# Performance work log

Hardware: AMD Instinct MI355X
Metric: run time of the kernel (lower is better)

Reference implementation:

```python
import jax, jax.numpy as jnp
import numpy as np

B, CIN, COUT, K, H, W, NPTS = 8, 256, 256, 4, 128, 128, 512


def setup_inputs() -> dict:
    key = jax.random.key(0)
    ks = jax.random.split(key, 9)
    inp = {
        'input': jax.random.normal(ks[0], (B, CIN, H, W), dtype=jnp.float32),
        'ax': jax.random.uniform(ks[1], (B, NPTS), dtype=jnp.float32) * (W - 1),
        'ay': jax.random.uniform(ks[2], (B, NPTS), dtype=jnp.float32) * (H - 1),
        # 1x1 conv = matmul over channels
        'Wp': jax.random.normal(ks[3], (COUT, CIN), dtype=jnp.float32) * 0.02,
        'bp': jnp.zeros((COUT,), dtype=jnp.float32),
        'Woff': jax.random.normal(ks[4], (K, 2, CIN), dtype=jnp.float32) * 0.02,
        'boff': jnp.zeros((K, 2), dtype=jnp.float32),
        'Ww': jax.random.normal(ks[5], (K, CIN), dtype=jnp.float32) * 0.02,
        'bw': jnp.zeros((K,), dtype=jnp.float32),
    }
    return inp


def _bilinear_zeros(img, xs, ys):
    """grid_sample(mode='bilinear', padding_mode='zeros').
    img: [b, C, H, W]; xs, ys: [b, H, W] source pixel coords. Returns [b, H, W, C]."""
    b, C, h, w = img.shape
    img_hwc = jnp.transpose(img, (0, 2, 3, 1))  # [b, H, W, C]
    x0 = jnp.floor(xs)
    y0 = jnp.floor(ys)
    wx1 = xs - x0
    wy1 = ys - y0
    bidx = jnp.arange(b)[:, None, None]

    def corner(xi, yi, wgt):
        valid = (xi >= 0) & (xi < w) & (yi >= 0) & (yi < h)
        xc = jnp.clip(xi, 0, w - 1).astype(jnp.int32)
        yc = jnp.clip(yi, 0, h - 1).astype(jnp.int32)
        v = img_hwc[bidx, yc, xc]  # [b, H, W, C]
        return v * (jnp.where(valid, wgt, 0.0))[..., None]

    out = (corner(x0, y0, (1 - wx1) * (1 - wy1))
           + corner(x0 + 1, y0, wx1 * (1 - wy1))
           + corner(x0, y0 + 1, (1 - wx1) * wy1)
           + corner(x0 + 1, y0 + 1, wx1 * wy1))
    return out


def _forward(input, ax, ay, Wp, bp, Woff, boff, Ww, bw):
    b, c, h, w = input.shape
    k = Ww.shape[0]
    proj = jnp.einsum('bchw,oc->bohw', input, Wp) + bp[None, :, None, None]
    # k flow fields [k, b, 2, h, w]
    flows = jnp.einsum('bchw,koc->kbohw', input, Woff) + boff[:, None, :, None, None]
    logits = jnp.einsum('bchw,kc->bkhw', input, Ww) + bw[None, :, None, None]
    wts = jax.nn.softmax(logits, axis=1)  # [b, k, h, w]

    gx = jnp.arange(w, dtype=input.dtype)[None, None, :]
    gy = jnp.arange(h, dtype=input.dtype)[None, :, None]
    # torch normalization: n = 2*v/(dim-1)-1, then grid_sample(align_corners=False)
    # maps n -> ((n+1)*dim - 1)/2 = v*dim/(dim-1) - 0.5
    sx_scale = w / max(w - 1, 1)
    sy_scale = h / max(h - 1, 1)

    # gather sum_k wts_k * sampled_k at every pixel (loop over small fixed k)
    summed = jnp.zeros((b, h, w, proj.shape[1]), dtype=input.dtype)
    for i in range(k):
        sx = (gx + flows[i, :, 0]) * sx_scale - 0.5  # [b, h, w]
        sy = (gy + flows[i, :, 1]) * sy_scale - 0.5
        summed = summed + wts[:, i, :, :, None] * _bilinear_zeros(proj, sx, sy)

    # point gather: feat[num, :, id[1], id[0]] with id = trunc((ax, ay))
    ix = jnp.trunc(ax).astype(jnp.int32)  # width index
    iy = jnp.trunc(ay).astype(jnp.int32)  # height index
    out = summed[jnp.arange(b)[:, None], iy, ix]  # [b, num_pts, out_ch]
    return out


def reference(input, ax, ay, Wp, bp, Woff, boff, Ww, bw):
    return _forward(input, ax, ay, Wp, bp, Woff, boff, Ww, bw)
```

## Files before the change

### kernel.cpp

```cpp
#include <hip/hip_runtime.h>
#include <hip/hip_fp16.h>

#define B_      8
#define CIN_    256
#define COUT_   256
#define K_      4
#define H_      128
#define W_      128
#define NPTS_   512

#define NPTS_TOT_   (B_ * NPTS_)
#define T_BYTES_    ((size_t)B_ * H_ * W_ * CIN_ * sizeof(__half))
#define WTS_OFF_    T_BYTES_
#define SITES_OFF_  (WTS_OFF_   + (size_t)NPTS_TOT_ * 16 * 4)
#define WSUM_OFF_   (SITES_OFF_ + (size_t)NPTS_TOT_ * 16 * 4)
#define WS_NEED_    (WSUM_OFF_  + (size_t)NPTS_TOT_ * 4)

__global__ __launch_bounds__(256) void ka_kernel(
    const float* __restrict__ input,
    const float* __restrict__ ax,
    const float* __restrict__ ay,
    const float* __restrict__ Woff,
    const float* __restrict__ boff,
    const float* __restrict__ Ww,
    const float* __restrict__ bw,
    __half* __restrict__ T,
    float* __restrict__ wts_g,
    int*   __restrict__ sites_g,
    float* __restrict__ wsums_g)
{
    __shared__ float lt[32][129];
    __shared__ float xs[CIN_];
    __shared__ float dotv[12];
    __shared__ float wc16[16];

    const int bid = blockIdx.x;
    const int t   = threadIdx.x;

    if (bid < 8192) {
        const int b   = bid >> 10;
        const int r   = bid & 1023;
        const int h   = r >> 3;
        const int c0  = (r & 7) << 5;

        const int c = t >> 3;
        const int m = t & 7;
        const float* __restrict__ src = input + (((size_t)(b * CIN_ + c0 + c) * H_ + h) * W_);
        #pragma unroll
        for (int q = 0; q < 4; ++q) {
            const int w = m * 4 + q * 32;
            const float4 v = *reinterpret_cast<const float4*>(src + w);
            lt[c][w]     = v.x;
            lt[c][w + 1] = v.y;
            lt[c][w + 2] = v.z;
            lt[c][w + 3] = v.w;
        }
        __syncthreads();

        const int wph = t >> 2;
        const int j0  = (t & 3) << 3;
        #pragma unroll
        for (int g = 0; g < 2; ++g) {
            const int w = wph + (g << 6);
            unsigned int words[4];
            #pragma unroll
            for (int i = 0; i < 4; ++i) {
                __half2 h2 = __floats2half2_rn(lt[j0 + 2 * i][w], lt[j0 + 2 * i + 1][w]);
                words[i] = *reinterpret_cast<unsigned int*>(&h2);
            }
            __half* dst = T + (((size_t)(b * H_ + h) * W_ + w) * CIN_ + c0 + j0);
            *reinterpret_cast<uint4*>(dst) = make_uint4(words[0], words[1], words[2], words[3]);
        }
        return;
    }

    const int pt = bid - 8192;
    const int b  = pt >> 9;

    const int ix = (int)truncf(ax[pt]);
    const int iy = (int)truncf(ay[pt]);
    const float* __restrict__ chan = input + (size_t)b * (CIN_ * H_ * W_) + (size_t)t * (H_ * W_);

    xs[t] = chan[iy * W_ + ix];
    __syncthreads();

    const int wave = t >> 6;
    const int lane = t & 63;
    #pragma unroll
    for (int r = 0; r < 3; ++r) {
        const int d = wave * 3 + r;
        const float* __restrict__ row = (d < 8) ? (Woff + d * CIN_) : (Ww + (d - 8) * CIN_);
        float s = 0.f;
        #pragma unroll
        for (int q = 0; q < 4; ++q) {
            const int c = lane + q * 64;
            s = fmaf(xs[c], row[c], s);
        }
        #pragma unroll
        for (int off = 32; off > 0; off >>= 1)
            s += __shfl_down(s, off);
        if (lane == 0) dotv[d] = s;
    }
    __syncthreads();

    if (t < 4) {
        const int k = t;
        const float l0 = dotv[8]  + bw[0];
        const float l1 = dotv[9]  + bw[1];
        const float l2 = dotv[10] + bw[2];
        const float l3 = dotv[11] + bw[3];
        const float mx = fmaxf(fmaxf(l0, l1), fmaxf(l2, l3));
        const float e0 = expf(l0 - mx), e1 = expf(l1 - mx);
        const float e2 = expf(l2 - mx), e3 = expf(l3 - mx);
        const float ek = (k == 0) ? e0 : (k == 1) ? e1 : (k == 2) ? e2 : e3;
        const float wk = ek / (e0 + e1 + e2 + e3);

        const float scale = 128.0f / 127.0f;
        const float fx = dotv[2 * k]     + boff[2 * k];
        const float fy = dotv[2 * k + 1] + boff[2 * k + 1];
        const float sxv = ((float)ix + fx) * scale - 0.5f;
        const float syv = ((float)iy + fy) * scale - 0.5f;
        const float x0f = floorf(sxv), y0f = floorf(syv);
        const float wx1 = sxv - x0f, wy1 = syv - y0f;
        const int x0 = (int)x0f, y0 = (int)y0f;
        #pragma unroll
        for (int ci = 0; ci < 4; ++ci) {
            const int xi = x0 + (ci & 1);
            const int yi = y0 + (ci >> 1);
            const bool valid = (xi >= 0) & (xi < W_) & (yi >= 0) & (yi < H_);
            float wc = ((ci & 1) ? wx1 : 1.f - wx1) * ((ci >> 1) ? wy1 : 1.f - wy1) * wk;
            wc = valid ? wc : 0.f;
            const int xc = min(max(xi, 0), W_ - 1);
            const int yc = min(max(yi, 0), H_ - 1);
            const int idx = k * 4 + ci;
            wc16[idx] = wc;
            wts_g[pt * 16 + idx]   = wc;
            sites_g[pt * 16 + idx] = ((b * H_ + yc) * W_ + xc) * CIN_;
        }
    }
    __syncthreads();
    if (t == 0) {
        float s = 0.f;
        #pragma unroll
        for (int i = 0; i < 16; ++i) s += wc16[i];
        wsums_g[pt] = s;
    }
}

__global__ __launch_bounds__(512) void kb_kernel(
    const __half* __restrict__ T,
    const float* __restrict__ Wp,
    const float* __restrict__ bp,
    const float* __restrict__ wts_g,
    const int*   __restrict__ sites_g,
    const float* __restrict__ wsums_g,
    float* __restrict__ out)
{
    __shared__ float xsh[16][260];
    __shared__ float wtile[32 * 256];
    __shared__ float swts[16][16];
    __shared__ int   ssites[16][16];
    __shared__ float swsum[16];

    const int blk = blockIdx.x;
    const int p0g = blk << 4;
    const int tid = threadIdx.x;

    if (tid < 256) {
        swts[tid >> 4][tid & 15]   = wts_g[p0g * 16 + tid];
        ssites[tid >> 4][tid & 15] = sites_g[p0g * 16 + tid];
    } else if (tid < 256 + 16) {
        swsum[tid - 256] = wsums_g[p0g + (tid - 256)];
    }
    __syncthreads();

    {
        const int p   = tid >> 5;
        const int oct = tid & 31;
        const int c0  = oct << 3;
        float a[8] = {0.f, 0.f, 0.f, 0.f, 0.f, 0.f, 0.f, 0.f};
        #pragma unroll
        for (int s = 0; s < 16; ++s) {
            const float w = swts[p][s];
            const uint4 raw = *reinterpret_cast<const uint4*>(T + (size_t)ssites[p][s] + c0);
            const __half* hh = reinterpret_cast<const __half*>(&raw);
            #pragma unroll
            for (int j = 0; j < 8; ++j)
                a[j] = fmaf(w, __half2float(hh[j]), a[j]);
        }
        *reinterpret_cast<float4*>(&xsh[p][c0])     = make_float4(a[0], a[1], a[2], a[3]);
        *reinterpret_cast<float4*>(&xsh[p][c0 + 4]) = make_float4(a[4], a[5], a[6], a[7]);
    }
    __syncthreads();

    const int oq = tid & 63;
    const int pp = tid >> 6;
    const int o0 = oq << 2;
    const int p0 = pp << 1;

    const float4 bpv = *reinterpret_cast<const float4*>(bp + o0);
    const float ws0 = swsum[p0], ws1 = swsum[p0 + 1];
    float a00 = bpv.x * ws0, a01 = bpv.y * ws0, a02 = bpv.z * ws0, a03 = bpv.w * ws0;
    float a10 = bpv.x * ws1, a11 = bpv.y * ws1, a12 = bpv.z * ws1, a13 = bpv.w * ws1;

    for (int ch = 0; ch < 8; ++ch) {
        #pragma unroll
        for (int r = 0; r < 4; ++r) {
            const int idx = r * 512 + tid;
            const int c4  = idx & 7;
            const int o   = idx >> 3;
            const float4 v = *reinterpret_cast<const float4*>(Wp + (size_t)o * CIN_ + ch * 32 + c4 * 4);
            const float vv[4] = {v.x, v.y, v.z, v.w};
            #pragma unroll
            for (int m = 0; m < 4; ++m) {
                const int c  = c4 * 4 + m;
                const int os = (o >> 2) ^ (c & 7);
                wtile[c * 256 + (os << 2) + (o & 3)] = vv[m];
            }
        }
        __syncthreads();

        const int cb = ch * 32;
        #pragma unroll
        for (int cq = 0; cq < 8; ++cq) {
            const float4 x0 = *reinterpret_cast<const float4*>(&xsh[p0][cb + (cq << 2)]);
            const float4 x1 = *reinterpret_cast<const float4*>(&xsh[p0 + 1][cb + (cq << 2)]);
            const float x0a[4] = {x0.x, x0.y, x0.z, x0.w};
            const float x1a[4] = {x1.x, x1.y, x1.z, x1.w};
            #pragma unroll
            for (int m = 0; m < 4; ++m) {
                const int c = (cq << 2) + m;
                const float4 wv = *reinterpret_cast<const float4*>(
                    &wtile[c * 256 + ((oq ^ (c & 7)) << 2)]);
                const float xm0 = x0a[m], xm1 = x1a[m];
                a00 = fmaf(xm0, wv.x, a00); a01 = fmaf(xm0, wv.y, a01);
                a02 = fmaf(xm0, wv.z, a02); a03 = fmaf(xm0, wv.w, a03);
                a10 = fmaf(xm1, wv.x, a10); a11 = fmaf(xm1, wv.y, a11);
                a12 = fmaf(xm1, wv.z, a12); a13 = fmaf(xm1, wv.w, a13);
            }
        }
        __syncthreads();
    }

    float* o_row0 = out + (size_t)(p0g + p0) * COUT_ + o0;
    float* o_row1 = out + (size_t)(p0g + p0 + 1) * COUT_ + o0;
    *reinterpret_cast<float4*>(o_row0) = make_float4(a00, a01, a02, a03);
    *reinterpret_cast<float4*>(o_row1) = make_float4(a10, a11, a12, a13);
}

__global__ __launch_bounds__(256) void ple_point_kernel(
    const float* __restrict__ input, const float* __restrict__ ax,
    const float* __restrict__ ay, const float* __restrict__ Wp,
    const float* __restrict__ bp, const float* __restrict__ Woff,
    const float* __restrict__ boff, const float* __restrict__ Ww,
    const float* __restrict__ bw, float* __restrict__ out)
{
    const int gid = blockIdx.x;
    const int b   = gid >> 9;
    const int tid = threadIdx.x;

    __shared__ float xs[CIN_];
    __shared__ float dotv[12];

    const int ix = (int)truncf(ax[gid]);
    const int iy = (int)truncf(ay[gid]);
    const float* __restrict__ chan = input + (size_t)b * (CIN_ * H_ * W_) + (size_t)tid * (H_ * W_);

    xs[tid] = chan[iy * W_ + ix];
    __syncthreads();

    const int wave = tid >> 6;
    const int lane = tid & 63;
    #pragma unroll
    for (int r = 0; r < 3; ++r) {
        const int d = wave * 3 + r;
        const float* __restrict__ row = (d < 8) ? (Woff + d * CIN_) : (Ww + (d - 8) * CIN_);
        float s = 0.f;
        #pragma unroll
        for (int q = 0; q < 4; ++q) s = fmaf(xs[lane + q * 64], row[lane + q * 64], s);
        #pragma unroll
        for (int off = 32; off > 0; off >>= 1) s += __shfl_down(s, off);
        if (lane == 0) dotv[d] = s;
    }
    __syncthreads();

    float lg[K_];
    float mx = -1e30f;
    #pragma unroll
    for (int k = 0; k < K_; ++k) { lg[k] = dotv[8 + k] + bw[k]; mx = fmaxf(mx, lg[k]); }
    float se = 0.f;
    #pragma unroll
    for (int k = 0; k < K_; ++k) { lg[k] = expf(lg[k] - mx); se += lg[k]; }
    const float inv_se = 1.f / se;
    const float scale = 128.0f / 127.0f;

    float xacc = 0.f, wsum = 0.f;
    #pragma unroll
    for (int k = 0; k < K_; ++k) {
        const float wk = lg[k] * inv_se;
        const float fx = dotv[2 * k] + boff[2 * k];
        const float fy = dotv[2 * k + 1] + boff[2 * k + 1];
        const float sxv = ((float)ix + fx) * scale - 0.5f;
        const float syv = ((float)iy + fy) * scale - 0.5f;
        const float x0f = floorf(sxv), y0f = floorf(syv);
        const float wx1 = sxv - x0f, wy1 = syv - y0f;
        const int x0 = (int)x0f, y0 = (int)y0f;
        const int x1 = x0 + 1, y1 = y0 + 1;
        const float w00 = (1.f - wx1) * (1.f - wy1) * wk;
        const float w10 = wx1 * (1.f - wy1) * wk;
        const float w01 = (1.f - wx1) * wy1 * wk;
        const float w11 = wx1 * wy1 * wk;
        const bool vx0 = (x0 >= 0) && (x0 < W_);
        const bool vx1 = (x1 >= 0) && (x1 < W_);
        if (y0 >= 0 && y0 < H_) {
            const float* rowp = chan + y0 * W_;
            if (vx0) { xacc = fmaf(w00, rowp[x0], xacc); wsum += w00; }
            if (vx1) { xacc = fmaf(w10, rowp[x1], xacc); wsum += w10; }
        }
        if (y1 >= 0 && y1 < H_) {
            const float* rowp = chan + y1 * W_;
            if (vx0) { xacc = fmaf(w01, rowp[x0], xacc); wsum += w01; }
            if (vx1) { xacc = fmaf(w11, rowp[x1], xacc); wsum += w11; }
        }
    }

    xs[tid] = xacc;
    __syncthreads();

    const float* __restrict__ wrow = Wp + tid * CIN_;
    float a0 = bp[tid] * wsum, a1 = 0.f, a2 = 0.f, a3 = 0.f;
    #pragma unroll 4
    for (int c = 0; c < CIN_; c += 4) {
        const float4 wv = *reinterpret_cast<const float4*>(wrow + c);
        a0 = fmaf(wv.x, xs[c], a0);
        a1 = fmaf(wv.y, xs[c + 1], a1);
        a2 = fmaf(wv.z, xs[c + 2], a2);
        a3 = fmaf(wv.w, xs[c + 3], a3);
    }
    out[(size_t)gid * COUT_ + tid] = (a0 + a1) + (a2 + a3);
}

extern "C" void kernel_launch(void* const* d_in, const int* in_sizes, int n_in,
                              void* d_out, int out_size, void* d_ws, size_t ws_size,
                              hipStream_t stream) {
    const float* input = (const float*)d_in[0];
    const float* ax    = (const float*)d_in[1];
    const float* ay    = (const float*)d_in[2];
    const float* Wp    = (const float*)d_in[3];
    const float* bp    = (const float*)d_in[4];
    const float* Woff  = (const float*)d_in[5];
    const float* boff  = (const float*)d_in[6];
    const float* Ww    = (const float*)d_in[7];
    const float* bw    = (const float*)d_in[8];
    float* out = (float*)d_out;

    if (ws_size >= WS_NEED_) {
        __half* T      = (__half*)d_ws;
        float*  wts_g  = (float*)((char*)d_ws + WTS_OFF_);
        int*    sites_g= (int*)  ((char*)d_ws + SITES_OFF_);
        float*  wsums_g= (float*)((char*)d_ws + WSUM_OFF_);

        ka_kernel<<<dim3(8192 + NPTS_TOT_), dim3(256), 0, stream>>>(
            input, ax, ay, Woff, boff, Ww, bw, T, wts_g, sites_g, wsums_g);
        kb_kernel<<<dim3(256), dim3(512), 0, stream>>>(
            T, Wp, bp, wts_g, sites_g, wsums_g, out);
    } else {
        ple_point_kernel<<<dim3(B_ * NPTS_), dim3(256), 0, stream>>>(
            input, ax, ay, Wp, bp, Woff, boff, Ww, bw, out);
    }
}
```

Baseline: 72.26 us.

## Use bf16 MFMA for point projection matmul and split output channels across blocks

Replaces the scalar FP32 FMA projection in the second kernel with bf16 MFMA 16x16x32 instructions, converting the gathered features and Wp tiles to bf16 in shared memory. The grid doubles so each block handles half the output channels, which adds parallelism but repeats the per-point gather of sampled features in both halves. Using bf16 lowers the precision of the projection.

```diff
diff --git a/kernel.cpp b/kernel.cpp
--- a/kernel.cpp
+++ b/kernel.cpp
@@ -15,6 +15,16 @@
 #define SITES_OFF_  (WTS_OFF_   + (size_t)NPTS_TOT_ * 16 * 4)
 #define WSUM_OFF_   (SITES_OFF_ + (size_t)NPTS_TOT_ * 16 * 4)
 #define WS_NEED_    (WSUM_OFF_  + (size_t)NPTS_TOT_ * 4)
+
+typedef __attribute__((ext_vector_type(8))) short short8v;
+typedef __attribute__((ext_vector_type(4))) float f32x4;
+
+__device__ __forceinline__ unsigned int bf16pair(float a, float b) {
+    unsigned int ua = __float_as_uint(a), ub = __float_as_uint(b);
+    ua = (ua + 0x7FFFu + ((ua >> 16) & 1u)) >> 16;
+    ub = (ub + 0x7FFFu + ((ub >> 16) & 1u)) >> 16;
+    return ua | (ub << 16);
+}
 
 __global__ __launch_bounds__(256) void ka_kernel(
     const float* __restrict__ input,
@@ -156,14 +166,16 @@
     const float* __restrict__ wsums_g,
     float* __restrict__ out)
 {
-    __shared__ float xsh[16][260];
-    __shared__ float wtile[32 * 256];
+    __shared__ float xsh[16][268];
+    __shared__ unsigned short wb[128 * 40];
     __shared__ float swts[16][16];
     __shared__ int   ssites[16][16];
     __shared__ float swsum[16];
 
     const int blk = blockIdx.x;
-    const int p0g = blk << 4;
+    const int pg  = blk >> 1;
+    const int nh  = blk & 1;
+    const int p0g = pg << 4;
     const int tid = threadIdx.x;
 
     if (tid < 256) {
@@ -183,69 +195,61 @@
         for (int s = 0; s < 16; ++s) {
             const float w = swts[p][s];
             const uint4 raw = *reinterpret_cast<const uint4*>(T + (size_t)ssites[p][s] + c0);
-            const __half* hh = reinterpret_cast<const __half*>(&raw);
+            const __half* hv = reinterpret_cast<const __half*>(&raw);
             #pragma unroll
             for (int j = 0; j < 8; ++j)
-                a[j] = fmaf(w, __half2float(hh[j]), a[j]);
+                a[j] = fmaf(w, __half2float(hv[j]), a[j]);
         }
         *reinterpret_cast<float4*>(&xsh[p][c0])     = make_float4(a[0], a[1], a[2], a[3]);
         *reinterpret_cast<float4*>(&xsh[p][c0 + 4]) = make_float4(a[4], a[5], a[6], a[7]);
     }
     __syncthreads();
 
-    const int oq = tid & 63;
-    const int pp = tid >> 6;
-    const int o0 = oq << 2;
-    const int p0 = pp << 1;
-
-    const float4 bpv = *reinterpret_cast<const float4*>(bp + o0);
-    const float ws0 = swsum[p0], ws1 = swsum[p0 + 1];
-    float a00 = bpv.x * ws0, a01 = bpv.y * ws0, a02 = bpv.z * ws0, a03 = bpv.w * ws0;
-    float a10 = bpv.x * ws1, a11 = bpv.y * ws1, a12 = bpv.z * ws1, a13 = bpv.w * ws1;
+    const int wave = tid >> 6;
+    const int lane = tid & 63;
+    const int mn   = lane & 15;
+    const int kb4  = lane >> 4;
+    const int n0   = nh * 128 + wave * 16;
+
+    const float bpv = bp[n0 + mn];
+    f32x4 acc;
+    acc[0] = bpv * swsum[kb4 * 4 + 0];
+    acc[1] = bpv * swsum[kb4 * 4 + 1];
+    acc[2] = bpv * swsum[kb4 * 4 + 2];
+    acc[3] = bpv * swsum[kb4 * 4 + 3];
 
     for (int ch = 0; ch < 8; ++ch) {
         #pragma unroll
-        for (int r = 0; r < 4; ++r) {
+        for (int r = 0; r < 2; ++r) {
             const int idx = r * 512 + tid;
-            const int c4  = idx & 7;
             const int o   = idx >> 3;
-            const float4 v = *reinterpret_cast<const float4*>(Wp + (size_t)o * CIN_ + ch * 32 + c4 * 4);
-            const float vv[4] = {v.x, v.y, v.z, v.w};
-            #pragma unroll
-            for (int m = 0; m < 4; ++m) {
-                const int c  = c4 * 4 + m;
-                const int os = (o >> 2) ^ (c & 7);
-                wtile[c * 256 + (os << 2) + (o & 3)] = vv[m];
-            }
+            const int q   = idx & 7;
+            const float4 v = *reinterpret_cast<const float4*>(
+                Wp + (size_t)(nh * 128 + o) * CIN_ + ch * 32 + q * 4);
+            unsigned int* w32 = reinterpret_cast<unsigned int*>(&wb[o * 40 + q * 4]);
+            w32[0] = bf16pair(v.x, v.y);
+            w32[1] = bf16pair(v.z, v.w);
         }
         __syncthreads();
 
-        const int cb = ch * 32;
-        #pragma unroll
-        for (int cq = 0; cq < 8; ++cq) {
-            const float4 x0 = *reinterpret_cast<const float4*>(&xsh[p0][cb + (cq << 2)]);
-            const float4 x1 = *reinterpret_cast<const float4*>(&xsh[p0 + 1][cb + (cq << 2)]);
-            const float x0a[4] = {x0.x, x0.y, x0.z, x0.w};
-            const float x1a[4] = {x1.x, x1.y, x1.z, x1.w};
-            #pragma unroll
-            for (int m = 0; m < 4; ++m) {
-                const int c = (cq << 2) + m;
-                const float4 wv = *reinterpret_cast<const float4*>(
-                    &wtile[c * 256 + ((oq ^ (c & 7)) << 2)]);
-                const float xm0 = x0a[m], xm1 = x1a[m];
-                a00 = fmaf(xm0, wv.x, a00); a01 = fmaf(xm0, wv.y, a01);
-                a02 = fmaf(xm0, wv.z, a02); a03 = fmaf(xm0, wv.w, a03);
-                a10 = fmaf(xm1, wv.x, a10); a11 = fmaf(xm1, wv.y, a11);
-                a12 = fmaf(xm1, wv.z, a12); a13 = fmaf(xm1, wv.w, a13);
-            }
-        }
+        const float* xrow = &xsh[mn][ch * 32 + kb4 * 8];
+        const float4 xa = *reinterpret_cast<const float4*>(xrow);
+        const float4 xb = *reinterpret_cast<const float4*>(xrow + 4);
+        union { unsigned int u[4]; short8v v; } af;
+        af.u[0] = bf16pair(xa.x, xa.y);
+        af.u[1] = bf16pair(xa.z, xa.w);
+        af.u[2] = bf16pair(xb.x, xb.y);
+        af.u[3] = bf16pair(xb.z, xb.w);
+
+        const short8v bf = *reinterpret_cast<const short8v*>(&wb[(wave * 16 + mn) * 40 + kb4 * 8]);
+
+        acc = __builtin_amdgcn_mfma_f32_16x16x32_bf16(af.v, bf, acc, 0, 0, 0);
         __syncthreads();
     }
 
-    float* o_row0 = out + (size_t)(p0g + p0) * COUT_ + o0;
-    float* o_row1 = out + (size_t)(p0g + p0 + 1) * COUT_ + o0;
-    *reinterpret_cast<float4*>(o_row0) = make_float4(a00, a01, a02, a03);
-    *reinterpret_cast<float4*>(o_row1) = make_float4(a10, a11, a12, a13);
+    #pragma unroll
+    for (int j = 0; j < 4; ++j)
+        out[(size_t)(p0g + kb4 * 4 + j) * COUT_ + n0 + mn] = acc[j];
 }
 
 __global__ __launch_bounds__(256) void ple_point_kernel(
@@ -331,11 +335,11 @@
     float a0 = bp[tid] * wsum, a1 = 0.f, a2 = 0.f, a3 = 0.f;
     #pragma unroll 4
     for (int c = 0; c < CIN_; c += 4) {
-        const float4 wv = *reinterpret_cast<const float4*>(wrow + c);
-        a0 = fmaf(wv.x, xs[c], a0);
-        a1 = fmaf(wv.y, xs[c + 1], a1);
-        a2 = fmaf(wv.z, xs[c + 2], a2);
-        a3 = fmaf(wv.w, xs[c + 3], a3);
+        const float4 wvv = *reinterpret_cast<const float4*>(wrow + c);
+        a0 = fmaf(wvv.x, xs[c], a0);
+        a1 = fmaf(wvv.y, xs[c + 1], a1);
+        a2 = fmaf(wvv.z, xs[c + 2], a2);
+        a3 = fmaf(wvv.w, xs[c + 3], a3);
     }
     out[(size_t)gid * COUT_ + tid] = (a0 + a1) + (a2 + a3);
 }
@@ -355,14 +359,14 @@
     float* out = (float*)d_out;
 
     if (ws_size >= WS_NEED_) {
-        __half* T      = (__half*)d_ws;
-        float*  wts_g  = (float*)((char*)d_ws + WTS_OFF_);
-        int*    sites_g= (int*)  ((char*)d_ws + SITES_OFF_);
-        float*  wsums_g= (float*)((char*)d_ws + WSUM_OFF_);
+        __half* T       = (__half*)d_ws;
+        float*  wts_g   = (float*)((char*)d_ws + WTS_OFF_);
+        int*    sites_g = (int*)  ((char*)d_ws + SITES_OFF_);
+        float*  wsums_g = (float*)((char*)d_ws + WSUM_OFF_);
 
         ka_kernel<<<dim3(8192 + NPTS_TOT_), dim3(256), 0, stream>>>(
             input, ax, ay, Woff, boff, Ww, bw, T, wts_g, sites_g, wsums_g);
-        kb_kernel<<<dim3(256), dim3(512), 0, stream>>>(
+        kb_kernel<<<dim3(512), dim3(512), 0, stream>>>(
             T, Wp, bp, wts_g, sites_g, wsums_g, out);
     } else {
         ple_point_kernel<<<dim3(B_ * NPTS_), dim3(256), 0, stream>>>(
```

Result: faster. 66.54 us (-7.9%).
